# Performance work log

Measured on AMD Instinct MI355X. Metric: run time of the kernel, lower is better.

The kernel has to match this reference:

```python
import jax, jax.numpy as jnp
import numpy as np

B, S, D = 8, 1024, 768
H = 12            # atten_heads
DH = D // H       # head dim = 64
F = 3072          # liner_dim
EPS = 1e-6


def _layer_norm(x, gamma, beta):
    mu = jnp.mean(x, axis=-1, keepdims=True)
    var = jnp.mean(jnp.square(x - mu), axis=-1, keepdims=True)
    return (x - mu) * jax.lax.rsqrt(var + EPS) * gamma + beta


def setup_inputs() -> dict:
    key = jax.random.key(0)
    ks = jax.random.split(key, 12)
    s = 0.02
    return {
        "x": jax.random.normal(ks[0], (B, S, D), jnp.float32),
        "Wq": jax.random.normal(ks[1], (D, D), jnp.float32) * s,
        "bq": jnp.zeros((D,), jnp.float32),
        "Wk": jax.random.normal(ks[2], (D, D), jnp.float32) * s,
        "bk": jnp.zeros((D,), jnp.float32),
        "Wv": jax.random.normal(ks[3], (D, D), jnp.float32) * s,
        "bv": jnp.zeros((D,), jnp.float32),
        "Wo": jax.random.normal(ks[4], (D, D), jnp.float32) * s,
        "bo": jnp.zeros((D,), jnp.float32),
        "g1": jnp.ones((D,), jnp.float32),
        "beta1": jnp.zeros((D,), jnp.float32),
        "g2": jnp.ones((D,), jnp.float32),
        "beta2": jnp.zeros((D,), jnp.float32),
        "W1": jax.random.normal(ks[5], (D, F), jnp.float32) * s,
        "b1": jnp.zeros((F,), jnp.float32),
        "W2": jax.random.normal(ks[6], (F, D), jnp.float32) * s,
        "b2": jnp.zeros((D,), jnp.float32),
    }


def reference(x, Wq, bq, Wk, bk, Wv, bv, Wo, bo, g1, beta1, g2, beta2, W1, b1, W2, b2):
    # pre-LN
    h = _layer_norm(x, g1, beta1)                       # [B,S,D]
    # QKV projections; tf.split(axis=-1)+concat(axis=0) == per-head view
    q = (h @ Wq + bq).reshape(B, S, H, DH)
    k = (h @ Wk + bk).reshape(B, S, H, DH)
    v = (h @ Wv + bv).reshape(B, S, H, DH)
    scale = 1.0 / jnp.sqrt(jnp.float32(DH))
    scores = jnp.einsum('bqhd,bkhd->bhqk', q, k) * scale  # [B,H,S,S]
    attn = jax.nn.softmax(scores, axis=-1)
    ctx = jnp.einsum('bhqk,bkhd->bqhd', attn, v).reshape(B, S, D)
    attn_out = ctx @ Wo + bo
    x2 = attn_out + x                                    # residual (dropout=0 at eval)
    # MLP block with exact (erf) GELU, as keras.activations.gelu default
    y = _layer_norm(x2, g2, beta2)
    y = jax.nn.gelu(y @ W1 + b1, approximate=False)
    y = y @ W2 + b2
    return x2 + y
```

## Files before the change

kernel.cpp:

```cpp
#include <hip/hip_runtime.h>
#include <stdint.h>

__device__ __forceinline__ float b2f(uint16_t u) {
    union { uint32_t i; float f; } v; v.i = ((uint32_t)u) << 16; return v.f;
}
__device__ __forceinline__ float b2f_lo(uint32_t u) {
    union { uint32_t i; float f; } v; v.i = u << 16; return v.f;
}
__device__ __forceinline__ float b2f_hi(uint32_t u) {
    union { uint32_t i; float f; } v; v.i = u & 0xFFFF0000u; return v.f;
}
__device__ __forceinline__ uint16_t f2b(float f) {
    union { float f; uint32_t i; } v; v.f = f;
    uint32_t r = v.i + 0x7FFF + ((v.i >> 16) & 1);
    return (uint16_t)(r >> 16);
}

typedef short  fragAB __attribute__((ext_vector_type(8)));
typedef float  fragC  __attribute__((ext_vector_type(4)));

#define MFMA(a, b, c) __builtin_amdgcn_mfma_f32_16x16x32_bf16((a), (b), (c), 0, 0, 0)

__device__ __forceinline__ void gload_lds16(const uint16_t* g, uint16_t* l) {
    __builtin_amdgcn_global_load_lds(
        (const __attribute__((address_space(1))) void*)g,
        (__attribute__((address_space(3))) void*)l, 16, 0, 0);
}

__global__ void detect_kernel(const uint16_t* __restrict__ g1, int* __restrict__ flag) {
    if (threadIdx.x == 0 && blockIdx.x == 0)
        flag[0] = (g1[0] == 0x3F80) ? 0 : 1;
}

__global__ __launch_bounds__(256) void convert_small_kernel(
    const void* p0, const void* p1, const void* p2, const void* p3, const void* p4,
    const void* p5, const void* p6, const void* p7, const void* p8, const void* p9,
    uint16_t* __restrict__ out, const int* __restrict__ flag)
{
    const int f = *flag;
    const void* p; int n; int off;
    switch (blockIdx.x) {
        case 0: p = p0; n = 768;  off = 0;    break;
        case 1: p = p1; n = 768;  off = 768;  break;
        case 2: p = p2; n = 768;  off = 1536; break;
        case 3: p = p3; n = 768;  off = 2304; break;
        case 4: p = p4; n = 768;  off = 3072; break;
        case 5: p = p5; n = 768;  off = 3840; break;
        case 6: p = p6; n = 768;  off = 4608; break;
        case 7: p = p7; n = 768;  off = 5376; break;
        case 8: p = p8; n = 3072; off = 6144; break;
        default: p = p9; n = 768; off = 9216; break;
    }
    uint16_t* o = out + off;
    for (int i = threadIdx.x; i < n; i += 256)
        o[i] = f ? f2b(((const float*)p)[i]) : ((const uint16_t*)p)[i];
}

__global__ __launch_bounds__(256) void transpose_kernel(
    const void* __restrict__ in, uint16_t* __restrict__ out, int R, int C,
    const int* __restrict__ flag)
{
    __shared__ uint16_t tile[32][33];
    const int f  = *flag;
    const int tx = threadIdx.x & 31;
    const int ty = threadIdx.x >> 5;
    const int r0 = blockIdx.y * 32, c0 = blockIdx.x * 32;
    #pragma unroll
    for (int i = 0; i < 32; i += 8) {
        size_t idx = (size_t)(r0 + ty + i) * C + c0 + tx;
        tile[ty + i][tx] = f ? f2b(((const float*)in)[idx]) : ((const uint16_t*)in)[idx];
    }
    __syncthreads();
    #pragma unroll
    for (int i = 0; i < 32; i += 8)
        out[(size_t)(c0 + ty + i) * R + r0 + tx] = tile[tx][ty + i];
}

__global__ __launch_bounds__(256) void convert_ln_kernel(
    const void* __restrict__ xraw, const int* __restrict__ flag,
    const uint16_t* __restrict__ g, const uint16_t* __restrict__ beta,
    uint16_t* __restrict__ xb, uint16_t* __restrict__ out)
{
    const int lane = threadIdx.x & 63;
    const int wave = threadIdx.x >> 6;
    const int row  = blockIdx.x * 4 + wave;
    uint32_t* xrow = (uint32_t*)(xb + (size_t)row * 768);
    float v[12];
    if (*flag) {
        const float2* xr = (const float2*)((const float*)xraw + (size_t)row * 768);
        #pragma unroll
        for (int i = 0; i < 6; i++) {
            float2 t = xr[i * 64 + lane];
            uint16_t a = f2b(t.x), b = f2b(t.y);
            xrow[i * 64 + lane] = (uint32_t)a | ((uint32_t)b << 16);
            v[2 * i] = b2f(a); v[2 * i + 1] = b2f(b);
        }
    } else {
        const uint32_t* xr = (const uint32_t*)xraw + (size_t)row * 384;
        #pragma unroll
        for (int i = 0; i < 6; i++) {
            uint32_t u = xr[i * 64 + lane];
            xrow[i * 64 + lane] = u;
            v[2 * i] = b2f_lo(u); v[2 * i + 1] = b2f_hi(u);
        }
    }
    float sum = 0.f, sq = 0.f;
    #pragma unroll
    for (int j = 0; j < 12; j++) { sum += v[j]; sq += v[j] * v[j]; }
    #pragma unroll
    for (int off = 32; off > 0; off >>= 1) {
        sum += __shfl_xor(sum, off);
        sq  += __shfl_xor(sq, off);
    }
    const float invn = 1.0f / 768.0f;
    float mu  = sum * invn;
    float var = sq * invn - mu * mu;
    float rs  = rsqrtf(var + 1e-6f);
    uint32_t* orow = (uint32_t*)(out + (size_t)row * 768);
    const uint32_t* gp = (const uint32_t*)g;
    const uint32_t* bp = (const uint32_t*)beta;
    #pragma unroll
    for (int i = 0; i < 6; i++) {
        int p = i * 64 + lane;
        uint32_t gu = gp[p], bu = bp[p];
        float o0 = (v[2 * i]     - mu) * rs * b2f_lo(gu) + b2f_lo(bu);
        float o1 = (v[2 * i + 1] - mu) * rs * b2f_hi(gu) + b2f_hi(bu);
        orow[p] = (uint32_t)f2b(o0) | ((uint32_t)f2b(o1) << 16);
    }
}

__global__ __launch_bounds__(256) void finish_ln_kernel(
    const uint16_t* __restrict__ pa, const uint16_t* __restrict__ pb,
    const uint16_t* __restrict__ bias, const uint16_t* __restrict__ res,
    const uint16_t* __restrict__ g, const uint16_t* __restrict__ beta,
    uint16_t* __restrict__ x2, uint16_t* __restrict__ out)
{
    const int lane = threadIdx.x & 63;
    const int wave = threadIdx.x >> 6;
    const int row  = blockIdx.x * 4 + wave;
    const uint32_t* par = (const uint32_t*)pa  + (size_t)row * 384;
    const uint32_t* pbr = (const uint32_t*)pb  + (size_t)row * 384;
    const uint32_t* rr  = (const uint32_t*)res + (size_t)row * 384;
    const uint32_t* bb  = (const uint32_t*)bias;
    uint32_t* x2r = (uint32_t*)(x2 + (size_t)row * 768);
    float v[12];
    float sum = 0.f, sq = 0.f;
    #pragma unroll
    for (int i = 0; i < 6; i++) {
        int p = i * 64 + lane;
        uint32_t ua = par[p], ub = pbr[p], ur = rr[p], uc = bb[p];
        float s0 = b2f_lo(ua) + b2f_lo(ub) + b2f_lo(uc) + b2f_lo(ur);
        float s1 = b2f_hi(ua) + b2f_hi(ub) + b2f_hi(uc) + b2f_hi(ur);
        uint16_t q0 = f2b(s0), q1 = f2b(s1);
        x2r[p] = (uint32_t)q0 | ((uint32_t)q1 << 16);
        float a = b2f(q0), b = b2f(q1);
        v[2 * i] = a; v[2 * i + 1] = b;
        sum += a + b; sq += a * a + b * b;
    }
    #pragma unroll
    for (int off = 32; off > 0; off >>= 1) {
        sum += __shfl_xor(sum, off);
        sq  += __shfl_xor(sq, off);
    }
    const float invn = 1.0f / 768.0f;
    float mu  = sum * invn;
    float var = sq * invn - mu * mu;
    float rs  = rsqrtf(var + 1e-6f);
    uint32_t* orow = (uint32_t*)(out + (size_t)row * 768);
    const uint32_t* gp = (const uint32_t*)g;
    const uint32_t* bp = (const uint32_t*)beta;
    #pragma unroll
    for (int i = 0; i < 6; i++) {
        int p = i * 64 + lane;
        uint32_t gu = gp[p], bu = bp[p];
        float o0 = (v[2 * i]     - mu) * rs * b2f_lo(gu) + b2f_lo(bu);
        float o1 = (v[2 * i + 1] - mu) * rs * b2f_hi(gu) + b2f_hi(bu);
        orow[p] = (uint32_t)f2b(o0) | ((uint32_t)f2b(o1) << 16);
    }
}

__global__ __launch_bounds__(512, 2) void gemm256_kernel(
    const uint16_t* __restrict__ A, const uint16_t* __restrict__ Wt,
    const uint16_t* __restrict__ bias, uint16_t* __restrict__ out,
    uint16_t* __restrict__ outB, int M, int N, int K, int mode)
{
    __shared__ __align__(16) uint16_t lds[65536];

    const int tid  = threadIdx.x;
    const int lane = tid & 63;
    const int wave = tid >> 6;
    const int qrow = lane & 15;
    const int quad = lane >> 4;
    const int wm   = (wave >> 2) * 128;
    const int wn   = (wave & 3) * 64;

    const int m0 = blockIdx.y * 256;
    const int n0 = blockIdx.x * 256;
    const int slice = blockIdx.z;
    const int kLen = K / gridDim.z;
    const int kOff = slice * kLen;
    const int nt   = kLen >> 6;

    const int sRow  = lane >> 3;
    const int sColE = (((lane & 7) ^ sRow) << 3);
    const uint16_t* aS00 = A  + (size_t)(m0 +   0 + wave * 8 + sRow) * K + kOff + sColE;
    const uint16_t* aS01 = A  + (size_t)(m0 +  64 + wave * 8 + sRow) * K + kOff + sColE;
    const uint16_t* aS10 = A  + (size_t)(m0 + 128 + wave * 8 + sRow) * K + kOff + sColE;
    const uint16_t* aS11 = A  + (size_t)(m0 + 192 + wave * 8 + sRow) * K + kOff + sColE;
    const uint16_t* bS00 = Wt + (size_t)(n0 +   0 + wave * 8 + sRow) * K + kOff + sColE;
    const uint16_t* bS01 = Wt + (size_t)(n0 +  64 + wave * 8 + sRow) * K + kOff + sColE;
    const uint16_t* bS10 = Wt + (size_t)(n0 + 128 + wave * 8 + sRow) * K + kOff + sColE;
    const uint16_t* bS11 = Wt + (size_t)(n0 + 192 + wave * 8 + sRow) * K + kOff + sColE;

#define STAGE_A(kt, h) do { \
        uint16_t* _d = lds + (((kt) & 1) << 15) + (h) * 8192 + wave * 512; \
        gload_lds16(((h) ? aS10 : aS00) + (size_t)(kt) * 64, _d); \
        gload_lds16(((h) ? aS11 : aS01) + (size_t)(kt) * 64, _d + 4096); \
    } while (0)
#define STAGE_B(kt, h) do { \
        uint16_t* _d = lds + (((kt) & 1) << 15) + 16384 + (h) * 8192 + wave * 512; \
        gload_lds16(((h) ? bS10 : bS00) + (size_t)(kt) * 64, _d); \
        gload_lds16(((h) ? bS11 : bS01) + (size_t)(kt) * 64, _d + 4096); \
    } while (0)

    const int s7  = qrow & 7;
    const int pe0 = ((quad    ) ^ s7) << 3;
    const int pe1 = ((quad + 4) ^ s7) << 3;
    const int aRd = ((wm >> 7) << 13) + qrow * 64;
    const int bRd = 16384 + ((wn >> 7) << 13) + ((wn & 127) + qrow) * 64;

    fragC acc[8][4] = {};
    fragAB bfr[4][2];

    STAGE_A(0, 0); STAGE_A(0, 1);
    STAGE_B(0, 0); STAGE_B(0, 1);
    STAGE_B(1, 0); STAGE_B(1, 1);
    __asm__ volatile("s_waitcnt vmcnt(4)" ::: "memory");
    __builtin_amdgcn_s_barrier();

    for (int v = 0; v < nt; v += 2) {
        #pragma unroll
        for (int ph = 0; ph < 8; ++ph) {
            const int sub = ph >> 2;
            const int q   = ph & 3;
            const int kt  = v + sub;
            const int dOff = (kt & 1) << 15;
            if (q == 0) {
                #pragma unroll
                for (int n = 0; n < 4; ++n) {
                    bfr[n][0] = *(const fragAB*)(lds + dOff + bRd + n * 1024 + pe0);
                    bfr[n][1] = *(const fragAB*)(lds + dOff + bRd + n * 1024 + pe1);
                }
            }
            fragAB a0k0 = *(const fragAB*)(lds + dOff + aRd + (q * 32     ) * 64 + pe0);
            fragAB a0k1 = *(const fragAB*)(lds + dOff + aRd + (q * 32     ) * 64 + pe1);
            fragAB a1k0 = *(const fragAB*)(lds + dOff + aRd + (q * 32 + 16) * 64 + pe0);
            fragAB a1k1 = *(const fragAB*)(lds + dOff + aRd + (q * 32 + 16) * 64 + pe1);
            switch (ph) {
                case 0: STAGE_A(v + 1, 0); break;
                case 1: STAGE_A(v + 1, 1); break;
                case 2: if (v + 2 < nt) STAGE_B(v + 2, 0); break;
                case 3: if (v + 2 < nt) STAGE_B(v + 2, 1); break;
                case 4: if (v + 2 < nt) STAGE_A(v + 2, 0); break;
                case 5: if (v + 2 < nt) STAGE_A(v + 2, 1); break;
                case 6: if (v + 3 < nt) STAGE_B(v + 3, 0); break;
                case 7: if (v + 3 < nt) STAGE_B(v + 3, 1); break;
            }
            __builtin_amdgcn_s_barrier();
            __builtin_amdgcn_s_setprio(1);
            #pragma unroll
            for (int n = 0; n < 4; ++n) {
                acc[2 * q    ][n] = MFMA(a0k0, bfr[n][0], acc[2 * q    ][n]);
                acc[2 * q    ][n] = MFMA(a0k1, bfr[n][1], acc[2 * q    ][n]);
                acc[2 * q + 1][n] = MFMA(a1k0, bfr[n][0], acc[2 * q + 1][n]);
                acc[2 * q + 1][n] = MFMA(a1k1, bfr[n][1], acc[2 * q + 1][n]);
            }
            __builtin_amdgcn_s_setprio(0);
            if (ph == 3 || ph == 7) {
                if (v + 2 < nt) { __asm__ volatile("s_waitcnt vmcnt(4)" ::: "memory"); }
                else            { __asm__ volatile("s_waitcnt vmcnt(0)" ::: "memory"); }
            }
            __builtin_amdgcn_s_barrier();
        }
    }
#undef STAGE_A
#undef STAGE_B

    __syncthreads();

    uint16_t* po = (mode == 7 && slice) ? outB : out;
    uint16_t* eb = lds + wave * 1152;
    float bvv[4];
    if (mode != 7) {
        #pragma unroll
        for (int ni = 0; ni < 4; ni++) bvv[ni] = b2f(bias[n0 + wn + ni * 16 + qrow]);
    }
    const int er = lane >> 2, ec = (lane & 3) * 16;
    #pragma unroll
    for (int mi = 0; mi < 8; mi++) {
        #pragma unroll
        for (int ni = 0; ni < 4; ni++) {
            #pragma unroll
            for (int r = 0; r < 4; r++) {
                float v = acc[mi][ni][r];
                if (mode != 7) {
                    v += bvv[ni];
                    if (mode == 2) {
                        float arg = v * (1.5957691216f + 0.0713548163f * v * v);
                        v = v * __builtin_amdgcn_rcpf(1.0f + __expf(-arg));
                    }
                }
                eb[(quad * 4 + r) * 72 + ni * 16 + qrow] = f2b(v);
            }
        }
        __asm__ volatile("s_waitcnt lgkmcnt(0)" ::: "memory");
        uint16_t* dst = po + (size_t)(m0 + wm + mi * 16 + er) * N + n0 + wn + ec;
        *(int4*)dst       = *(const int4*)&eb[er * 72 + ec];
        *(int4*)(dst + 8) = *(const int4*)&eb[er * 72 + ec + 8];
        __asm__ volatile("" ::: "memory");
    }
}

__global__ __launch_bounds__(256) void finish_kernel(
    const uint16_t* __restrict__ pa, const uint16_t* __restrict__ pb,
    const uint16_t* __restrict__ bias, const uint16_t* __restrict__ res,
    void* __restrict__ out, const int* __restrict__ flag)
{
    const int i = (blockIdx.x * 256 + threadIdx.x) * 4;
    const int n = i % 768;
    ushort4 av = *(const ushort4*)(pa + i);
    ushort4 pv = *(const ushort4*)(pb + i);
    ushort4 rv = *(const ushort4*)(res + i);
    ushort4 cv = *(const ushort4*)(bias + n);
    float o0 = b2f(av.x) + b2f(pv.x) + b2f(cv.x) + b2f(rv.x);
    float o1 = b2f(av.y) + b2f(pv.y) + b2f(cv.y) + b2f(rv.y);
    float o2 = b2f(av.z) + b2f(pv.z) + b2f(cv.z) + b2f(rv.z);
    float o3 = b2f(av.w) + b2f(pv.w) + b2f(cv.w) + b2f(rv.w);
    if (flag && *flag) {
        *(float4*)((float*)out + i) = make_float4(o0, o1, o2, o3);
    } else {
        ushort4 ov;
        ov.x = f2b(o0); ov.y = f2b(o1); ov.z = f2b(o2); ov.w = f2b(o3);
        *(ushort4*)((uint16_t*)out + i) = ov;
    }
}

__global__ __launch_bounds__(256) void attn_kernel(
    const uint16_t* __restrict__ QKV, uint16_t* __restrict__ ctx)
{
    __shared__ __align__(16) uint16_t Ks[128 * 72];
    __shared__ __align__(16) uint16_t Vs[64 * 72];
    __shared__ __align__(16) uint16_t Ps[4][2][16 * 72];
    const int tid  = threadIdx.x;
    const int lane = tid & 63;
    const int wave = tid >> 6;
    const int qrow = lane & 15;
    const int quad = lane >> 4;

    const int flat = blockIdx.x + 8 * blockIdx.y;
    const int xcd = flat & 7, local = flat >> 3;
    const int bh = xcd * 12 + (local >> 3);
    const int b  = bh / 12, hh = bh % 12;
    const int q0blk = (local & 7) * 128;
    const int q0 = q0blk + wave * 32;

    const uint16_t* base = QKV + (size_t)b * 1024 * 2304;
    const uint16_t* Qp = base + hh * 64;
    const uint16_t* Kp = base + 768 + hh * 64;
    const uint16_t* Vp = base + 1536 + hh * 64;

    const int srow = tid >> 2;
    const int scol = (tid & 3) * 16;
    const int pkey = srow ^ scol;

    fragAB qf[2][2];
    #pragma unroll
    for (int qq = 0; qq < 2; qq++)
        #pragma unroll
        for (int c = 0; c < 2; c++)
            qf[qq][c] = *(const fragAB*)(Qp + (size_t)(q0 + qq * 16 + qrow) * 2304 + c * 32 + quad * 8);

    fragC ao[2][4] = {};
    float lsum[2][4] = {};

    for (int kk = 0; kk < 1024; kk += 64) {
        __syncthreads();
        *(int4*)&Ks[srow * 72 + scol]     = *(const int4*)(Kp + (size_t)(kk + srow) * 2304 + scol);
        *(int4*)&Ks[srow * 72 + scol + 8] = *(const int4*)(Kp + (size_t)(kk + srow) * 2304 + scol + 8);
        {
            union { int4 q[2]; uint16_t u[16]; } t;
            t.q[0] = *(const int4*)(Vp + (size_t)(kk + srow) * 2304 + scol);
            t.q[1] = *(const int4*)(Vp + (size_t)(kk + srow) * 2304 + scol + 8);
            #pragma unroll
            for (int j = 0; j < 16; j++)
                Vs[(scol + j) * 72 + pkey] = t.u[j];
        }
        __syncthreads();

        fragC sc[2][4] = {};
        #pragma unroll
        for (int g = 0; g < 4; g++) {
            fragAB kf0 = *(const fragAB*)&Ks[(g * 16 + qrow) * 72 + quad * 8];
            fragAB kf1 = *(const fragAB*)&Ks[(g * 16 + qrow) * 72 + 32 + quad * 8];
            #pragma unroll
            for (int qq = 0; qq < 2; qq++) {
                sc[qq][g] = MFMA(qf[qq][0], kf0, sc[qq][g]);
                sc[qq][g] = MFMA(qf[qq][1], kf1, sc[qq][g]);
            }
        }

        #pragma unroll
        for (int qq = 0; qq < 2; qq++)
            #pragma unroll
            for (int g = 0; g < 4; g++)
                #pragma unroll
                for (int r = 0; r < 4; r++) {
                    float p = __expf(fminf(sc[qq][g][r] * 0.125f, 20.0f));
                    lsum[qq][r] += p;
                    Ps[wave][qq][(quad * 4 + r) * 72 + g * 16 + qrow] = f2b(p);
                }
        __syncthreads();

        fragAB pf[2][2];
        #pragma unroll
        for (int qq = 0; qq < 2; qq++)
            #pragma unroll
            for (int c = 0; c < 2; c++)
                pf[qq][c] = *(const fragAB*)&Ps[wave][qq][qrow * 72 + c * 32 + quad * 8];

        #pragma unroll
        for (int f = 0; f < 4; f++) {
            fragAB vf0 = *(const fragAB*)&Vs[(f * 16 + qrow) * 72 + ((0 + quad * 8) ^ (f * 16))];
            fragAB vf1 = *(const fragAB*)&Vs[(f * 16 + qrow) * 72 + ((32 + quad * 8) ^ (f * 16))];
            #pragma unroll
            for (int qq = 0; qq < 2; qq++) {
                ao[qq][f] = MFMA(pf[qq][0], vf0, ao[qq][f]);
                ao[qq][f] = MFMA(pf[qq][1], vf1, ao[qq][f]);
            }
        }
    }

    float inv[2][4];
    #pragma unroll
    for (int qq = 0; qq < 2; qq++)
        #pragma unroll
        for (int r = 0; r < 4; r++) {
            float s = lsum[qq][r];
            #pragma unroll
            for (int off = 1; off < 16; off <<= 1) s += __shfl_xor(s, off);
            inv[qq][r] = 1.0f / s;
        }

    #pragma unroll
    for (int qq = 0; qq < 2; qq++)
        #pragma unroll
        for (int f = 0; f < 4; f++)
            #pragma unroll
            for (int r = 0; r < 4; r++)
                Ks[(wave * 32 + qq * 16 + quad * 4 + r) * 72 + f * 16 + qrow] =
                    f2b(ao[qq][f][r] * inv[qq][r]);
    __syncthreads();
    {
        const int row = tid >> 1, half = tid & 1;
        uint16_t* dst = ctx + (size_t)(b * 1024 + q0blk + row) * 768 + hh * 64 + half * 32;
        const uint16_t* src = &Ks[row * 72 + half * 32];
        *(int4*)dst        = *(const int4*)src;
        *(int4*)(dst + 8)  = *(const int4*)(src + 8);
        *(int4*)(dst + 16) = *(const int4*)(src + 16);
        *(int4*)(dst + 24) = *(const int4*)(src + 24);
    }
}

extern "C" void kernel_launch(void* const* d_in, const int* in_sizes, int n_in,
                              void* d_out, int out_size, void* d_ws, size_t ws_size,
                              hipStream_t stream)
{
    (void)in_sizes; (void)n_in; (void)out_size; (void)ws_size;
    const void* x_raw  = d_in[0];
    const void* Wq_raw = d_in[1];
    const void* bq_raw = d_in[2];
    const void* Wk_raw = d_in[3];
    const void* bk_raw = d_in[4];
    const void* Wv_raw = d_in[5];
    const void* bv_raw = d_in[6];
    const void* Wo_raw = d_in[7];
    const void* bo_raw = d_in[8];
    const void* g1_raw = d_in[9];
    const void* be1_raw= d_in[10];
    const void* g2_raw = d_in[11];
    const void* be2_raw= d_in[12];
    const void* W1_raw = d_in[13];
    const void* b1_raw = d_in[14];
    const void* W2_raw = d_in[15];
    const void* b2_raw = d_in[16];

    uint8_t* ws = (uint8_t*)d_ws;
    const size_t SZ = (size_t)8192 * 768 * 2;
    uint16_t* xb    = (uint16_t*)(ws);
    uint16_t* h1    = (uint16_t*)(ws + SZ);
    uint16_t* QKVb  = (uint16_t*)(ws + 2 * SZ);
    uint16_t* ctx   = (uint16_t*)(ws + 5 * SZ);
    uint16_t* pWa   = (uint16_t*)(ws + 2 * SZ);
    uint16_t* pWb   = (uint16_t*)(ws + SZ);
    uint16_t* x2    = (uint16_t*)(ws + 5 * SZ);
    uint16_t* ln2   = (uint16_t*)(ws + 6 * SZ);
    uint16_t* y1    = (uint16_t*)(ws);
    uint16_t* pMa   = (uint16_t*)(ws + 4 * SZ);
    uint16_t* pMb   = (uint16_t*)(ws + 6 * SZ);
    uint8_t*  wts   = ws + 7 * SZ;
    uint16_t* WqkvT = (uint16_t*)(wts);
    uint16_t* WoT   = (uint16_t*)(wts + 3 * 1179648);
    uint16_t* W1T   = (uint16_t*)(wts + 4 * 1179648);
    uint16_t* W2T   = (uint16_t*)(wts + 4 * 1179648 + 4718592);
    uint16_t* smallv = (uint16_t*)(wts + 4 * 1179648 + 2 * 4718592);
    int* flag = (int*)(wts + 4 * 1179648 + 2 * 4718592 + 9984 * 2);
    uint16_t* G1   = smallv + 0,    *BE1 = smallv + 768;
    uint16_t* G2   = smallv + 1536, *BE2 = smallv + 2304;
    uint16_t* BQKV = smallv + 3072;
    uint16_t* BO   = smallv + 5376;
    uint16_t* B1   = smallv + 6144, *B2 = smallv + 9216;

    dim3 blk(256);
    dim3 blk2(512);
    detect_kernel<<<1, 64, 0, stream>>>((const uint16_t*)g1_raw, flag);
    convert_small_kernel<<<10, blk, 0, stream>>>(g1_raw, be1_raw, g2_raw, be2_raw,
        bq_raw, bk_raw, bv_raw, bo_raw, b1_raw, b2_raw, smallv, flag);

    transpose_kernel<<<dim3(24, 24), blk, 0, stream>>>(Wq_raw, WqkvT,              768, 768, flag);
    transpose_kernel<<<dim3(24, 24), blk, 0, stream>>>(Wk_raw, WqkvT + 589824,     768, 768, flag);
    transpose_kernel<<<dim3(24, 24), blk, 0, stream>>>(Wv_raw, WqkvT + 2 * 589824, 768, 768, flag);
    transpose_kernel<<<dim3(24, 24), blk, 0, stream>>>(Wo_raw, WoT, 768, 768, flag);
    transpose_kernel<<<dim3(96, 24), blk, 0, stream>>>(W1_raw, W1T, 768, 3072, flag);
    transpose_kernel<<<dim3(24, 96), blk, 0, stream>>>(W2_raw, W2T, 3072, 768, flag);

    convert_ln_kernel<<<2048, blk, 0, stream>>>(x_raw, flag, G1, BE1, xb, h1);

    gemm256_kernel<<<dim3(9, 32), blk2, 0, stream>>>(h1, WqkvT, BQKV, QKVb, nullptr,
                                                     8192, 2304, 768, 0);

    attn_kernel<<<dim3(8, 96), blk, 0, stream>>>(QKVb, ctx);

    gemm256_kernel<<<dim3(3, 32, 2), blk2, 0, stream>>>(ctx, WoT, BO, pWa, pWb,
                                                        8192, 768, 768, 7);
    finish_ln_kernel<<<2048, blk, 0, stream>>>(pWa, pWb, BO, xb, G2, BE2, x2, ln2);

    gemm256_kernel<<<dim3(12, 32), blk2, 0, stream>>>(ln2, W1T, B1, y1, nullptr,
                                                      8192, 3072, 768, 2);

    gemm256_kernel<<<dim3(3, 32, 2), blk2, 0, stream>>>(y1, W2T, B2, pMa, pMb,
                                                        8192, 768, 3072, 7);
    finish_kernel<<<6144, blk, 0, stream>>>(pMa, pMb, B2, x2, d_out, flag);
}
```

Before: 297.4 us.

## Fuse weight prep launches into one kernel and swizzle GEMM blocks by XCD

Replaces the separate dtype-detect, small-vector conversion and six transpose launches with a single prep kernel, and computes the dtype check inline from g1 in each kernel. The GEMM block index is remapped so blocks that share the same M tile run on the same XCD, aiming for better L2 reuse of A and weight tiles. Fewer launches cut launch gaps, while the remap changes block scheduling order and adds a little index arithmetic.

```diff
diff --git a/kernel.cpp b/kernel.cpp
--- a/kernel.cpp
+++ b/kernel.cpp
@@ -27,48 +27,67 @@
         (__attribute__((address_space(3))) void*)l, 16, 0, 0);
 }
 
-__global__ void detect_kernel(const uint16_t* __restrict__ g1, int* __restrict__ flag) {
-    if (threadIdx.x == 0 && blockIdx.x == 0)
-        flag[0] = (g1[0] == 0x3F80) ? 0 : 1;
-}
-
-__global__ __launch_bounds__(256) void convert_small_kernel(
-    const void* p0, const void* p1, const void* p2, const void* p3, const void* p4,
-    const void* p5, const void* p6, const void* p7, const void* p8, const void* p9,
-    uint16_t* __restrict__ out, const int* __restrict__ flag)
-{
-    const int f = *flag;
-    const void* p; int n; int off;
-    switch (blockIdx.x) {
-        case 0: p = p0; n = 768;  off = 0;    break;
-        case 1: p = p1; n = 768;  off = 768;  break;
-        case 2: p = p2; n = 768;  off = 1536; break;
-        case 3: p = p3; n = 768;  off = 2304; break;
-        case 4: p = p4; n = 768;  off = 3072; break;
-        case 5: p = p5; n = 768;  off = 3840; break;
-        case 6: p = p6; n = 768;  off = 4608; break;
-        case 7: p = p7; n = 768;  off = 5376; break;
-        case 8: p = p8; n = 3072; off = 6144; break;
-        default: p = p9; n = 768; off = 9216; break;
-    }
-    uint16_t* o = out + off;
-    for (int i = threadIdx.x; i < n; i += 256)
-        o[i] = f ? f2b(((const float*)p)[i]) : ((const uint16_t*)p)[i];
-}
-
-__global__ __launch_bounds__(256) void transpose_kernel(
-    const void* __restrict__ in, uint16_t* __restrict__ out, int R, int C,
-    const int* __restrict__ flag)
+__device__ __forceinline__ int dtype_is_f32(const void* g1raw) {
+    return ((const uint16_t*)g1raw)[0] != 0x3F80;
+}
+
+__global__ __launch_bounds__(256) void prep_kernel(
+    const void* Wq, const void* Wk, const void* Wv, const void* Wo,
+    const void* W1, const void* W2,
+    uint16_t* __restrict__ WqkvT, uint16_t* __restrict__ WoT,
+    uint16_t* __restrict__ W1T, uint16_t* __restrict__ W2T,
+    const void* g1, const void* be1, const void* g2, const void* be2,
+    const void* bq, const void* bk, const void* bv, const void* bo,
+    const void* b1, const void* b2, uint16_t* __restrict__ smallv)
 {
     __shared__ uint16_t tile[32][33];
-    const int f  = *flag;
+    const int f = dtype_is_f32(g1);
+    const int idx = blockIdx.x;
+
+    if (idx >= 6912) {
+        const void* p; int n; int off;
+        switch (idx - 6912) {
+            case 0: p = g1;  n = 768;  off = 0;    break;
+            case 1: p = be1; n = 768;  off = 768;  break;
+            case 2: p = g2;  n = 768;  off = 1536; break;
+            case 3: p = be2; n = 768;  off = 2304; break;
+            case 4: p = bq;  n = 768;  off = 3072; break;
+            case 5: p = bk;  n = 768;  off = 3840; break;
+            case 6: p = bv;  n = 768;  off = 4608; break;
+            case 7: p = bo;  n = 768;  off = 5376; break;
+            case 8: p = b1;  n = 3072; off = 6144; break;
+            default: p = b2; n = 768;  off = 9216; break;
+        }
+        uint16_t* o = smallv + off;
+        for (int i = threadIdx.x; i < n; i += 256)
+            o[i] = f ? f2b(((const float*)p)[i]) : ((const uint16_t*)p)[i];
+        return;
+    }
+
+    const void* in; uint16_t* out; int R, C, bx, by;
+    if (idx < 2304) {
+        const int w = idx / 576, t = idx % 576;
+        bx = t % 24; by = t / 24; R = 768; C = 768;
+        switch (w) {
+            case 0:  in = Wq; out = WqkvT;              break;
+            case 1:  in = Wk; out = WqkvT + 589824;     break;
+            case 2:  in = Wv; out = WqkvT + 2 * 589824; break;
+            default: in = Wo; out = WoT;                break;
+        }
+    } else if (idx < 4608) {
+        const int t = idx - 2304;
+        bx = t % 96; by = t / 96; in = W1; out = W1T; R = 768; C = 3072;
+    } else {
+        const int t = idx - 4608;
+        bx = t % 24; by = t / 24; in = W2; out = W2T; R = 3072; C = 768;
+    }
     const int tx = threadIdx.x & 31;
     const int ty = threadIdx.x >> 5;
-    const int r0 = blockIdx.y * 32, c0 = blockIdx.x * 32;
+    const int r0 = by * 32, c0 = bx * 32;
     #pragma unroll
     for (int i = 0; i < 32; i += 8) {
-        size_t idx = (size_t)(r0 + ty + i) * C + c0 + tx;
-        tile[ty + i][tx] = f ? f2b(((const float*)in)[idx]) : ((const uint16_t*)in)[idx];
+        size_t p = (size_t)(r0 + ty + i) * C + c0 + tx;
+        tile[ty + i][tx] = f ? f2b(((const float*)in)[p]) : ((const uint16_t*)in)[p];
     }
     __syncthreads();
     #pragma unroll
@@ -77,7 +96,7 @@
 }
 
 __global__ __launch_bounds__(256) void convert_ln_kernel(
-    const void* __restrict__ xraw, const int* __restrict__ flag,
+    const void* __restrict__ xraw, const void* __restrict__ g1raw,
     const uint16_t* __restrict__ g, const uint16_t* __restrict__ beta,
     uint16_t* __restrict__ xb, uint16_t* __restrict__ out)
 {
@@ -86,7 +105,7 @@
     const int row  = blockIdx.x * 4 + wave;
     uint32_t* xrow = (uint32_t*)(xb + (size_t)row * 768);
     float v[12];
-    if (*flag) {
+    if (dtype_is_f32(g1raw)) {
         const float2* xr = (const float2*)((const float*)xraw + (size_t)row * 768);
         #pragma unroll
         for (int i = 0; i < 6; i++) {
@@ -194,10 +213,15 @@
     const int wm   = (wave >> 2) * 128;
     const int wn   = (wave & 3) * 64;
 
-    const int m0 = blockIdx.y * 256;
-    const int n0 = blockIdx.x * 256;
-    const int slice = blockIdx.z;
-    const int kLen = K / gridDim.z;
+    const int gx = gridDim.x, gy = gridDim.y, gz = gridDim.z;
+    const int flat = blockIdx.x + gx * (blockIdx.y + gy * blockIdx.z);
+    const int xcd = flat & 7;
+    const int local = flat >> 3;
+    const int n0 = (local % gx) * 256;
+    const int mz = (local / gx) * 8 + xcd;
+    const int m0 = (mz % gy) * 256;
+    const int slice = mz / gy;
+    const int kLen = K / gz;
     const int kOff = slice * kLen;
     const int nt   = kLen >> 6;
 
@@ -324,7 +348,7 @@
 __global__ __launch_bounds__(256) void finish_kernel(
     const uint16_t* __restrict__ pa, const uint16_t* __restrict__ pb,
     const uint16_t* __restrict__ bias, const uint16_t* __restrict__ res,
-    void* __restrict__ out, const int* __restrict__ flag)
+    void* __restrict__ out, const void* __restrict__ g1raw)
 {
     const int i = (blockIdx.x * 256 + threadIdx.x) * 4;
     const int n = i % 768;
@@ -336,7 +360,7 @@
     float o1 = b2f(av.y) + b2f(pv.y) + b2f(cv.y) + b2f(rv.y);
     float o2 = b2f(av.z) + b2f(pv.z) + b2f(cv.z) + b2f(rv.z);
     float o3 = b2f(av.w) + b2f(pv.w) + b2f(cv.w) + b2f(rv.w);
-    if (flag && *flag) {
+    if (dtype_is_f32(g1raw)) {
         *(float4*)((float*)out + i) = make_float4(o0, o1, o2, o3);
     } else {
         ushort4 ov;
@@ -513,7 +537,6 @@
     uint16_t* W1T   = (uint16_t*)(wts + 4 * 1179648);
     uint16_t* W2T   = (uint16_t*)(wts + 4 * 1179648 + 4718592);
     uint16_t* smallv = (uint16_t*)(wts + 4 * 1179648 + 2 * 4718592);
-    int* flag = (int*)(wts + 4 * 1179648 + 2 * 4718592 + 9984 * 2);
     uint16_t* G1   = smallv + 0,    *BE1 = smallv + 768;
     uint16_t* G2   = smallv + 1536, *BE2 = smallv + 2304;
     uint16_t* BQKV = smallv + 3072;
@@ -522,18 +545,14 @@
 
     dim3 blk(256);
     dim3 blk2(512);
-    detect_kernel<<<1, 64, 0, stream>>>((const uint16_t*)g1_raw, flag);
-    convert_small_kernel<<<10, blk, 0, stream>>>(g1_raw, be1_raw, g2_raw, be2_raw,
-        bq_raw, bk_raw, bv_raw, bo_raw, b1_raw, b2_raw, smallv, flag);
-
-    transpose_kernel<<<dim3(24, 24), blk, 0, stream>>>(Wq_raw, WqkvT,              768, 768, flag);
-    transpose_kernel<<<dim3(24, 24), blk, 0, stream>>>(Wk_raw, WqkvT + 589824,     768, 768, flag);
-    transpose_kernel<<<dim3(24, 24), blk, 0, stream>>>(Wv_raw, WqkvT + 2 * 589824, 768, 768, flag);
-    transpose_kernel<<<dim3(24, 24), blk, 0, stream>>>(Wo_raw, WoT, 768, 768, flag);
-    transpose_kernel<<<dim3(96, 24), blk, 0, stream>>>(W1_raw, W1T, 768, 3072, flag);
-    transpose_kernel<<<dim3(24, 96), blk, 0, stream>>>(W2_raw, W2T, 3072, 768, flag);
-
-    convert_ln_kernel<<<2048, blk, 0, stream>>>(x_raw, flag, G1, BE1, xb, h1);
+
+    prep_kernel<<<6922, blk, 0, stream>>>(
+        Wq_raw, Wk_raw, Wv_raw, Wo_raw, W1_raw, W2_raw,
+        WqkvT, WoT, W1T, W2T,
+        g1_raw, be1_raw, g2_raw, be2_raw,
+        bq_raw, bk_raw, bv_raw, bo_raw, b1_raw, b2_raw, smallv);
+
+    convert_ln_kernel<<<2048, blk, 0, stream>>>(x_raw, g1_raw, G1, BE1, xb, h1);
 
     gemm256_kernel<<<dim3(9, 32), blk2, 0, stream>>>(h1, WqkvT, BQKV, QKVb, nullptr,
                                                      8192, 2304, 768, 0);
@@ -549,5 +568,5 @@
 
     gemm256_kernel<<<dim3(3, 32, 2), blk2, 0, stream>>>(y1, W2T, B2, pMa, pMb,
                                                         8192, 768, 3072, 7);
-    finish_kernel<<<6144, blk, 0, stream>>>(pMa, pMb, B2, x2, d_out, flag);
-}
+    finish_kernel<<<6144, blk, 0, stream>>>(pMa, pMb, B2, x2, d_out, g1_raw);
+}
```

Result: faster. 274.0 us (median of 2 runs) (-7.9%).
